# Kernel tuning notes

Measured on AMD Instinct MI355X. Metric: run time of the kernel, lower is better.

## Reference

```python
import jax, jax.numpy as jnp
import numpy as np

# dims (match init_kwargs)
L, CH, PIX, PAT, RC, BD, OUT, B = 64, 16, 256, 64, 32, 64, 10, 256


def setup_inputs() -> dict:
    key = jax.random.key(0)
    ks = jax.random.split(key, 10)
    sd = lambda k, shape, s: jax.random.normal(k, shape, dtype=jnp.float32) * s
    # stds calibrated so each bond-contraction step has ~unit gain (quimb's
    # MPS_rand_state produces normalized states; this mirrors that stability)
    chi_first = sd(ks[0], (RC, CH), 0.70)               # (r, phys)
    chi_mid   = sd(ks[1], (L - 2, RC, RC, CH), 0.70)    # (site, l, r, phys)
    chi_last  = sd(ks[2], (RC, CH, OUT), 0.70 * 0.01)   # (l, phys, out) -- new_ind rand_strength=0.01
    psi_first = sd(ks[3], (BD, PIX), 1.0 / 32)
    psi_mid   = sd(ks[4], (L - 2, BD, BD, PIX), 1.0 / 32)
    psi_last  = sd(ks[5], (BD, PIX), 1.0 / 32)
    phi_first = sd(ks[6], (BD, PAT), 0.125)
    phi_mid   = sd(ks[7], (L - 2, BD, BD, PAT), 0.125)
    phi_last  = sd(ks[8], (BD, PAT), 0.125)
    x = jax.random.normal(ks[9], (B, PAT, PIX, CH), dtype=jnp.float32)
    return dict(x=x, chi_first=chi_first, chi_mid=chi_mid, chi_last=chi_last,
                psi_first=psi_first, psi_mid=psi_mid, psi_last=psi_last,
                phi_first=phi_first, phi_mid=phi_mid, phi_last=phi_last)


def _batched_chain(first, mid, vecs):
    # first: (bond, p); mid: (L-2, l, r, p); vecs: (L, B, p)
    v0 = jnp.einsum('rp,bp->br', first, vecs[0])
    def step(v, wu):
        W, u = wu
        return jnp.einsum('bl,lrp,bp->br', v, W, u), None
    v, _ = jax.lax.scan(step, v0, (mid, vecs[1:-1]))
    return v  # (B, bond)


def reference(x, chi_first, chi_mid, chi_last, psi_first, psi_mid, psi_last,
              phi_first, phi_mid, phi_last):
    Bn, nP, nPix, nCh = x.shape
    idx = jnp.arange(L) % nP  # site -> patch index (identity when L == n_patches)
    # per-site input vectors (contract phys legs of each MPS with data)
    vch = jnp.transpose(x.mean(axis=-2)[:, idx, :], (1, 0, 2))  # (L, B, CH)
    vpx = jnp.transpose(x.mean(axis=-1)[:, idx, :], (1, 0, 2))  # (L, B, PIX)
    # chi chain -> (B, out)
    v_chi = _batched_chain(chi_first, chi_mid, vch)
    chi_out = jnp.einsum('bl,lpo,bp->bo', v_chi, chi_last, vch[-1])
    # psi chain -> (B,)
    v_psi = _batched_chain(psi_first, psi_mid, vpx)
    psi_val = jnp.einsum('bl,lp,bp->b', v_psi, psi_last, vpx[-1])
    # phi chain: one-hot patch positions, batch-independent -> scalar
    e = jax.nn.one_hot(idx, nP, dtype=x.dtype)  # (L, PAT)
    u0 = jnp.einsum('rp,p->r', phi_first, e[0])
    def pstep(v, wu):
        W, u = wu
        return jnp.einsum('l,lrp,p->r', v, W, u), None
    u, _ = jax.lax.scan(pstep, u0, (phi_mid, e[1:-1]))
    phi_val = jnp.einsum('l,lp,p->', u, phi_last, e[-1])
    return chi_out * (psi_val * phi_val)[:, None]  # (B, out)
```

## Files before the change

### kernel.cpp

```cpp
#include <hip/hip_runtime.h>


static inline int imin(int a, int b) { return a < b ? a : b; }

typedef __attribute__((ext_vector_type(4))) float f32x4;
typedef _Float16 f16;
typedef __attribute__((ext_vector_type(8))) _Float16 f16x8;

__global__ __launch_bounds__(256) void k_reduce_x(const float* __restrict__ x,
                                                  float* __restrict__ vch,
                                                  float* __restrict__ vpx,
                                                  f16* __restrict__ vpxf,
                                                  const float* __restrict__ phi_mid,
                                                  float* __restrict__ slices) {
  if (blockIdx.x >= 16384) {
    int i = blockIdx.x - 16384;
    int t = threadIdx.x;
    #pragma unroll
    for (int k = 0; k < 16; ++k) {
      int idx = t + k * 256;
      slices[(size_t)i * 4096 + idx] = phi_mid[((size_t)i * 4096 + idx) * 64 + (i + 1)];
    }
    return;
  }
  int bp = blockIdx.x;
  int b = bp >> 6, s = bp & 63;
  int q = threadIdx.x;
  const float* row = x + ((size_t)bp << 12) + q * 16;
  float4 r0 = *(const float4*)(row);
  float4 r1 = *(const float4*)(row + 4);
  float4 r2 = *(const float4*)(row + 8);
  float4 r3 = *(const float4*)(row + 12);
  float csum = r0.x + r0.y + r0.z + r0.w + r1.x + r1.y + r1.z + r1.w
             + r2.x + r2.y + r2.z + r2.w + r3.x + r3.y + r3.z + r3.w;
  float val = csum * (1.0f / 16.0f);
  if (vpx && (s == 0 || s == 63)) vpx[((size_t)s * 256 + b) * 256 + q] = val;
  if (vpxf && s >= 1 && s <= 62) {
    size_t fa = (size_t)s * 65536
              + (((size_t)(q >> 5) * 16 + (b >> 4)) * 64 + (((q >> 3) & 3) * 16 + (b & 15))) * 8
              + (q & 7);
    vpxf[fa] = (f16)val;
  }

  __shared__ float sc[256][20];
  *(float4*)&sc[q][0]  = r0;
  *(float4*)&sc[q][4]  = r1;
  *(float4*)&sc[q][8]  = r2;
  *(float4*)&sc[q][12] = r3;
  __syncthreads();
  int c = q & 15, g = q >> 4;
  float ps = 0.f;
  #pragma unroll
  for (int k = 0; k < 16; ++k) ps += sc[g * 16 + k][c];
  __shared__ float p2[16][17];
  p2[g][c] = ps;
  __syncthreads();
  if (q < 16) {
    float s2 = 0.f;
    #pragma unroll
    for (int k = 0; k < 16; ++k) s2 += p2[k][q];
    vch[((size_t)s * 256 + b) * 16 + q] = s2 * (1.0f / 256.0f);
  }
}

__device__ __forceinline__ void psi_gemm_tile(const float* __restrict__ W,
                                              const f16* __restrict__ Afg,
                                              f16* __restrict__ Mz,
                                              int lr0, int t,
                                              unsigned char* smem) {
  typedef f16 BArr[2][2][4][64][8];
  BArr& Bf = *reinterpret_cast<BArr*>(smem);
  int lane = t & 63, w = t >> 6;
  int row = t >> 3, kg = t & 7;
  float4 svA0, svA1, svB0, svB1;

  #define LOADPA(p) do {                                                     \
    const float* src = W + (size_t)(lr0 + row) * 256 + ((p) << 6) + kg * 8;  \
    svA0 = *(const float4*)src;                                              \
    svA1 = *(const float4*)(src + 4);                                        \
  } while (0)
  #define LOADPB(p) do {                                                     \
    const float* src = W + (size_t)(lr0 + row) * 256 + ((p) << 6) + kg * 8;  \
    svB0 = *(const float4*)src;                                              \
    svB1 = *(const float4*)(src + 4);                                        \
  } while (0)
  #define WRITEPA(d) do {                                                    \
    float xs[8] = {svA0.x, svA0.y, svA0.z, svA0.w, svA1.x, svA1.y, svA1.z, svA1.w}; \
    f16x8 fv;                                                                \
    _Pragma("unroll")                                                        \
    for (int i = 0; i < 8; ++i) fv[i] = (f16)xs[i];                          \
    int ck = kg >> 2, nt = row >> 4, ln = ((kg & 3) << 4) | (row & 15);      \
    *(f16x8*)&Bf[d][ck][nt][ln][0] = fv;                                     \
  } while (0)
  #define WRITEPB(d) do {                                                    \
    float xs[8] = {svB0.x, svB0.y, svB0.z, svB0.w, svB1.x, svB1.y, svB1.z, svB1.w}; \
    f16x8 fv;                                                                \
    _Pragma("unroll")                                                        \
    for (int i = 0; i < 8; ++i) fv[i] = (f16)xs[i];                          \
    int ck = kg >> 2, nt = row >> 4, ln = ((kg & 3) << 4) | (row & 15);      \
    *(f16x8*)&Bf[d][ck][nt][ln][0] = fv;                                     \
  } while (0)
  #define LOADA(slot, chunk) do {                                            \
    _Pragma("unroll")                                                        \
    for (int mi = 0; mi < 2; ++mi) {                                         \
      size_t fo = ((size_t)(chunk) * 16 + (w * 2 + mi)) * 512 + (size_t)lane * 8; \
      Af[slot][mi] = *(const f16x8*)(Afg + fo);                              \
    }                                                                        \
  } while (0)
  #define COMPUTE(p) do {                                                    \
    _Pragma("unroll")                                                        \
    for (int c = 0; c < 2; ++c) {                                            \
      const int chunk = (p) * 2 + c;                                         \
      const int cur = chunk & 1, nxt = (chunk + 1) & 1;                      \
      if (chunk < 7) LOADA(nxt, chunk + 1);                                  \
      _Pragma("unroll")                                                      \
      for (int n = 0; n < 4; ++n) {                                          \
        f16x8 bf = *(const f16x8*)&Bf[(p) & 1][c][n][lane][0];               \
        _Pragma("unroll")                                                    \
        for (int mi = 0; mi < 2; ++mi) {                                     \
          acc[mi][n] = __builtin_amdgcn_mfma_f32_16x16x32_f16(Af[cur][mi], bf, acc[mi][n], 0, 0, 0); \
        }                                                                    \
      }                                                                      \
    }                                                                        \
  } while (0)

  f32x4 acc[2][4];
  #pragma unroll
  for (int i = 0; i < 2; ++i)
    #pragma unroll
    for (int j = 0; j < 4; ++j) acc[i][j] = (f32x4){0.f, 0.f, 0.f, 0.f};
  f16x8 Af[2][2];

  LOADA(0, 0);
  LOADPA(0);
  LOADPB(1);
  WRITEPA(0);
  __syncthreads();
  LOADPA(2);
  COMPUTE(0);
  WRITEPB(1);
  __syncthreads();
  LOADPB(3);
  COMPUTE(1);
  WRITEPA(0);
  __syncthreads();
  COMPUTE(2);
  WRITEPB(1);
  __syncthreads();
  COMPUTE(3);
  __syncthreads();
  #undef LOADPA
  #undef LOADPB
  #undef WRITEPA
  #undef WRITEPB
  #undef LOADA
  #undef COMPUTE

  int rg = lane >> 4, cidx = lane & 15;
  f16 (*T)[72] = reinterpret_cast<f16 (*)[72]>(smem);
  #pragma unroll
  for (int pass = 0; pass < 2; ++pass) {
    if ((w >> 2) == pass) {
      #pragma unroll
      for (int mi = 0; mi < 2; ++mi) {
        int rowb = (((w & 3) * 2 + mi) * 16) + rg * 4;
        #pragma unroll
        for (int n = 0; n < 4; ++n) {
          #pragma unroll
          for (int r = 0; r < 4; ++r) {
            T[rowb + r][n * 16 + cidx] = (f16)acc[mi][n][r];
          }
        }
      }
    }
    __syncthreads();
    int boff = pass * 128;
    #pragma unroll
    for (int k = 0; k < 2; ++k) {
      int f = t + k * 512;
      int b2 = f >> 3;
      int l8 = (f & 7) * 8;
      *(f16x8*)(Mz + ((size_t)(boff + b2)) * 4096 + lr0 + l8) =
          *(const f16x8*)&T[b2][l8];
    }
    __syncthreads();
  }
}

__global__ __launch_bounds__(512) void k_mega_A(const float* __restrict__ psi_mid,
                                                const f16* __restrict__ vpxf,
                                                f16* __restrict__ M,
                                                const float* __restrict__ chi_mid,
                                                const float* __restrict__ vch,
                                                float* __restrict__ Tc,
                                                const float* __restrict__ slices,
                                                const float* __restrict__ phi_first,
                                                const float* __restrict__ phi_last,
                                                float* __restrict__ phiv) {
  int bx = blockIdx.x;
  int t = threadIdx.x;
  if (bx == 0) {
    int r = t & 63, g = t >> 6;
    __shared__ float u[64];
    __shared__ float part[8][64];
    __shared__ float red[64];
    if (t < 64) u[t] = phi_first[t * 64];
    __syncthreads();
    for (int i2 = 0; i2 < 62; ++i2) {
      float sum = 0.f;
      #pragma unroll
      for (int j = 0; j < 8; ++j) {
        int l = g * 8 + j;
        sum += u[l] * slices[(size_t)i2 * 4096 + l * 64 + r];
      }
      part[g][r] = sum;
      __syncthreads();
      if (g == 0) u[r] = part[0][r] + part[1][r] + part[2][r] + part[3][r]
                       + part[4][r] + part[5][r] + part[6][r] + part[7][r];
      __syncthreads();
    }
    if (t < 64) red[t] = u[t] * phi_last[t * 64 + 63];
    __syncthreads();
    if (t == 0) {
      float s = 0.f;
      for (int l = 0; l < 64; ++l) s += red[l];
      *phiv = s;
    }
  } else if (bx <= 496) {
    int i = bx - 1;
    int z = i >> 3;
    int b0 = (i & 7) * 32;
    __shared__ float uv[32][16];
    if (t < 128) {
      int idx = t * 4;
      int b = idx >> 4, c = idx & 15;
      *(float4*)&uv[b][c] = *(const float4*)(vch + ((size_t)(z + 1) * 256 + b0 + b) * 16 + c);
    }
    __syncthreads();
    #pragma unroll
    for (int k = 0; k < 2; ++k) {
      int idx = t + k * 512;
      int r = idx >> 5, l = idx & 31;
      const float* Wp = chi_mid + ((size_t)z * 1024 + l * 32 + r) * 16;
      float4 w0 = *(const float4*)(Wp);
      float4 w1 = *(const float4*)(Wp + 4);
      float4 w2 = *(const float4*)(Wp + 8);
      float4 w3 = *(const float4*)(Wp + 12);
      for (int b = 0; b < 32; ++b) {
        const float* u = uv[b];
        float d = w0.x * u[0] + w0.y * u[1] + w0.z * u[2] + w0.w * u[3]
                + w1.x * u[4] + w1.y * u[5] + w1.z * u[6] + w1.w * u[7]
                + w2.x * u[8] + w2.y * u[9] + w2.z * u[10] + w2.w * u[11]
                + w3.x * u[12] + w3.y * u[13] + w3.z * u[14] + w3.w * u[15];
        Tc[((size_t)z * 256 + b0 + b) * 1024 + idx] = d;
      }
    }
  } else {
    int idx = bx - 497;
    int z = idx >> 6;
    int lr0 = (idx & 63) * 64;
    __shared__ __align__(16) unsigned char smem[18432];
    psi_gemm_tile(psi_mid + (size_t)z * 4096 * 256,
                  vpxf + (size_t)(z + 1) * 65536,
                  M + (size_t)z * 256 * 4096, lr0, t, smem);
  }
}

__global__ __launch_bounds__(512) void k_mega_B(const float* __restrict__ psi_mid,
                                                const f16* __restrict__ vpxf,
                                                f16* __restrict__ M,
                                                const float* __restrict__ Tc,
                                                const float* __restrict__ vpx,
                                                const float* __restrict__ vch,
                                                const float* __restrict__ psi_first,
                                                const float* __restrict__ chi_first,
                                                const float* __restrict__ chi_last,
                                                float* __restrict__ vpsi,
                                                float* __restrict__ chiout) {
  int bx = blockIdx.x;
  int t = threadIdx.x;
  if (bx < 256) {
    int b = bx;
    int r = t & 63, g = t >> 6;
    __shared__ float vsh[64];
    __shared__ float part[8][64];
    {
      const float* u0 = vpx + (size_t)b * 256;
      const float* pf = psi_first + r * 256 + g * 32;
      float s0 = 0.f;
      #pragma unroll
      for (int p = 0; p < 32; ++p) s0 += pf[p] * u0[g * 32 + p];
      part[g][r] = s0;
      __syncthreads();
      if (g == 0) {
        float sv = 0.f;
        #pragma unroll
        for (int k = 0; k < 8; ++k) sv += part[k][r];
        vsh[r] = sv;
      }
      __syncthreads();
    }
    #define QLOAD(buf, sc) do {                                                \
      const f16* Mb = M + ((size_t)(sc) * 256 + b) * 4096 + r;                 \
      _Pragma("unroll")                                                        \
      for (int j = 0; j < 8; ++j) buf[j] = (float)Mb[(size_t)(g * 8 + j) * 64]; \
    } while (0)
    #define QSTEP(buf) do {                                                    \
      float sum = 0.f;                                                         \
      _Pragma("unroll")                                                        \
      for (int j = 0; j < 8; ++j) sum += vsh[g * 8 + j] * buf[j];              \
      part[g][r] = sum;                                                        \
      __syncthreads();                                                         \
      if (g == 0) {                                                            \
        float sv = 0.f;                                                        \
        _Pragma("unroll")                                                      \
        for (int k = 0; k < 8; ++k) sv += part[k][r];                          \
        vsh[r] = sv;                                                           \
      }                                                                        \
      __syncthreads();                                                         \
    } while (0)
    float bufA[8], bufB[8];
    QLOAD(bufA, 0);
    #pragma unroll 1
    for (int sc = 0; sc < 36; sc += 2) {
      QLOAD(bufB, sc + 1);
      QSTEP(bufA);
      if (sc + 2 < 36) QLOAD(bufA, sc + 2);
      QSTEP(bufB);
    }
    #undef QLOAD
    #undef QSTEP
    if (g == 0) vpsi[b * 64 + r] = vsh[r];
  } else if (bx < 512) {
    if (t >= 64) return;
    int b = bx - 256;
    int lane = t;
    int r = lane & 31, h = lane >> 5;
    float v;
    {
      const float* u0 = vch + (size_t)b * 16;
      const float* cf = chi_first + r * 16;
      float s0 = 0.f;
      #pragma unroll
      for (int c = 0; c < 16; ++c) s0 += cf[c] * u0[c];
      v = s0;
    }
    #define CLOADX(buf, sc) do {                                               \
      const float* Mb = Tc + ((size_t)(sc) * 256 + b) * 1024 + r * 32 + h * 16; \
      *(float4*)&buf[0]  = *(const float4*)(Mb);                               \
      *(float4*)&buf[4]  = *(const float4*)(Mb + 4);                           \
      *(float4*)&buf[8]  = *(const float4*)(Mb + 8);                           \
      *(float4*)&buf[12] = *(const float4*)(Mb + 12);                          \
    } while (0)
    #define CSTEPX(buf) do {                                                   \
      float s0 = 0.f, s1 = 0.f;                                                \
      _Pragma("unroll")                                                        \
      for (int j = 0; j < 8; ++j) {                                            \
        s0 += __shfl(v, h * 16 + 2 * j)     * buf[2 * j];                      \
        s1 += __shfl(v, h * 16 + 2 * j + 1) * buf[2 * j + 1];                  \
      }                                                                        \
      float sum = s0 + s1;                                                     \
      sum += __shfl_xor(sum, 32);                                              \
      v = sum;                                                                 \
    } while (0)
    {
      float mjA[16], mjB[16];
      CLOADX(mjA, 0);
      #pragma unroll 1
      for (int sc = 0; sc < 62; sc += 2) {
        CLOADX(mjB, sc + 1);
        CSTEPX(mjA);
        if (sc + 2 < 62) CLOADX(mjA, sc + 2);
        CSTEPX(mjB);
      }
    }
    #undef CLOADX
    #undef CSTEPX
    const float* u63 = vch + ((size_t)63 * 256 + b) * 16;
    float uc[16];
    #pragma unroll
    for (int c = 0; c < 16; ++c) uc[c] = u63[c];
    for (int o = 0; o < 10; ++o) {
      const float* cl = chi_last + r * 16 * 10 + o;
      float wv = 0.f;
      #pragma unroll
      for (int c = 0; c < 16; ++c) wv += cl[c * 10] * uc[c];
      float p = v * wv;
      #pragma unroll
      for (int m = 32; m > 0; m >>= 1) p += __shfl_xor(p, m);
      if (lane == 0) chiout[b * 10 + o] = p * 0.5f;
    }
  } else {
    int idx = bx - 512;
    int z = 36 + (idx >> 6);
    int lr0 = (idx & 63) * 64;
    __shared__ __align__(16) unsigned char smem[18432];
    psi_gemm_tile(psi_mid + (size_t)z * 4096 * 256,
                  vpxf + (size_t)(z + 1) * 65536,
                  M + (size_t)z * 256 * 4096, lr0, t, smem);
  }
}

__global__ __launch_bounds__(64) void k_chain_tail(const f16* __restrict__ M,
                                                   const float* __restrict__ vpx,
                                                   const float* __restrict__ psi_last,
                                                   const float* __restrict__ chiout,
                                                   const float* __restrict__ phiv,
                                                   const float* __restrict__ vpsi,
                                                   float* __restrict__ out) {
  int b = blockIdx.x;
  int lane = threadIdx.x;
  float v = vpsi[b * 64 + lane];
  #define MLOAD(buf, sc) do {                                                \
    const f16* Mb = M + ((size_t)(36 + (sc)) * 256 + b) * 4096 + lane;       \
    _Pragma("unroll")                                                        \
    for (int l = 0; l < 64; ++l) buf[l] = (float)Mb[(size_t)l * 64];         \
  } while (0)
  #define MSTEP(buf) do {                                                    \
    float s0 = 0.f, s1 = 0.f, s2 = 0.f, s3 = 0.f;                            \
    _Pragma("unroll")                                                        \
    for (int l = 0; l < 16; ++l) {                                           \
      s0 += __shfl(v, 4 * l + 0) * buf[4 * l + 0];                           \
      s1 += __shfl(v, 4 * l + 1) * buf[4 * l + 1];                           \
      s2 += __shfl(v, 4 * l + 2) * buf[4 * l + 2];                           \
      s3 += __shfl(v, 4 * l + 3) * buf[4 * l + 3];                           \
    }                                                                        \
    v = (s0 + s1) + (s2 + s3);                                               \
  } while (0)
  {
    float mvA[64], mvB[64];
    MLOAD(mvA, 0);
    #pragma unroll 1
    for (int sc = 0; sc < 26; sc += 2) {
      MLOAD(mvB, sc + 1);
      MSTEP(mvA);
      if (sc + 2 < 26) MLOAD(mvA, sc + 2);
      MSTEP(mvB);
    }
  }
  #undef MLOAD
  #undef MSTEP
  float acc_p = 0.f;
  #pragma unroll
  for (int pp = 0; pp < 4; ++pp) {
    int p = pp * 64 + lane;
    float pl[64];
    #pragma unroll
    for (int l = 0; l < 64; ++l) pl[l] = psi_last[l * 256 + p];
    float s0 = 0.f, s1 = 0.f, s2 = 0.f, s3 = 0.f;
    #pragma unroll
    for (int l = 0; l < 16; ++l) {
      s0 += __shfl(v, 4 * l + 0) * pl[4 * l + 0];
      s1 += __shfl(v, 4 * l + 1) * pl[4 * l + 1];
      s2 += __shfl(v, 4 * l + 2) * pl[4 * l + 2];
      s3 += __shfl(v, 4 * l + 3) * pl[4 * l + 3];
    }
    float wv = (s0 + s1) + (s2 + s3);
    acc_p += wv * vpx[((size_t)63 * 256 + b) * 256 + p];
  }
  #pragma unroll
  for (int m = 32; m > 0; m >>= 1) acc_p += __shfl_xor(acc_p, m);
  if (lane < 10) out[b * 10 + lane] = chiout[b * 10 + lane] * acc_p * phiv[0];
}

__global__ __launch_bounds__(512) void k_psi_gemm(const float* __restrict__ psi_mid,
                                                  const f16* __restrict__ vpxf,
                                                  f16* __restrict__ M, int s0) {
  int z = blockIdx.z;
  int s = s0 + z;
  int lr0 = blockIdx.x * 64;
  __shared__ __align__(16) unsigned char smem[18432];
  psi_gemm_tile(psi_mid + (size_t)s * 4096 * 256,
                vpxf + (size_t)(s + 1) * 65536,
                M + (size_t)z * 256 * 4096, lr0, threadIdx.x, smem);
}

__global__ __launch_bounds__(256) void k_psi_chain(const f16* __restrict__ M,
                                                   const float* __restrict__ vpx,
                                                   const float* __restrict__ psi_first,
                                                   const float* __restrict__ psi_last,
                                                   float* __restrict__ vpsi,
                                                   float* __restrict__ psiv,
                                                   int nS, int isFirst, int isLast) {
  int b = blockIdx.x;
  int t = threadIdx.x;
  int r = t & 63, g = t >> 6;
  __shared__ float v[64];
  __shared__ float part[4][64];
  __shared__ float red[256];
  if (isFirst) {
    const float* u0 = vpx + (size_t)b * 256;
    float s0 = 0.f;
    for (int p = g * 64; p < g * 64 + 64; ++p) s0 += psi_first[r * 256 + p] * u0[p];
    part[g][r] = s0;
    __syncthreads();
    if (g == 0) v[r] = part[0][r] + part[1][r] + part[2][r] + part[3][r];
    __syncthreads();
  } else {
    if (g == 0) v[r] = vpsi[b * 64 + r];
    __syncthreads();
  }
  for (int sc = 0; sc < nS; ++sc) {
    const f16* Mb = M + ((size_t)sc * 256 + b) * 4096;
    float sum = 0.f;
    #pragma unroll
    for (int j = 0; j < 16; ++j) {
      int l = g * 16 + j;
      sum += v[l] * (float)Mb[l * 64 + r];
    }
    part[g][r] = sum;
    __syncthreads();
    if (g == 0) v[r] = part[0][r] + part[1][r] + part[2][r] + part[3][r];
    __syncthreads();
  }
  if (isLast) {
    float qv = 0.f;
    for (int l = 0; l < 64; ++l) qv += v[l] * psi_last[l * 256 + t];
    red[t] = qv * vpx[((size_t)63 * 256 + b) * 256 + t];
    __syncthreads();
    for (int off = 128; off > 0; off >>= 1) {
      if (t < off) red[t] += red[t + off];
      __syncthreads();
    }
    if (t == 0) psiv[b] = red[0];
  } else {
    if (g == 0) vpsi[b * 64 + r] = v[r];
  }
}

__device__ __forceinline__ void phi_chain_body(const float* __restrict__ slices,
                                               const float* __restrict__ phi_first,
                                               const float* __restrict__ phi_last,
                                               float* __restrict__ phiv) {
  int t = threadIdx.x;
  int r = t & 63, g = t >> 6;
  __shared__ float u[64];
  __shared__ float part[4][64];
  __shared__ float red[64];
  if (t < 64) u[t] = phi_first[t * 64];
  __syncthreads();
  for (int i = 0; i < 62; ++i) {
    float sum = 0.f;
    #pragma unroll
    for (int j = 0; j < 16; ++j) {
      int l = g * 16 + j;
      sum += u[l] * slices[(size_t)i * 4096 + l * 64 + r];
    }
    part[g][r] = sum;
    __syncthreads();
    if (g == 0) u[r] = part[0][r] + part[1][r] + part[2][r] + part[3][r];
    __syncthreads();
  }
  if (t < 64) red[t] = u[t] * phi_last[t * 64 + 63];
  __syncthreads();
  if (t == 0) {
    float s = 0.f;
    for (int l = 0; l < 64; ++l) s += red[l];
    *phiv = s;
  }
}

__global__ __launch_bounds__(256) void k_phi_chain(const float* __restrict__ slices,
                                                   const float* __restrict__ phi_first,
                                                   const float* __restrict__ phi_last,
                                                   float* __restrict__ phiv) {
  phi_chain_body(slices, phi_first, phi_last, phiv);
}

__global__ __launch_bounds__(256) void k_chi_gemm(const float* __restrict__ chi_mid,
                                                  const float* __restrict__ vch,
                                                  float* __restrict__ Tc, int s0,
                                                  int phiBlock,
                                                  const float* __restrict__ slices,
                                                  const float* __restrict__ phi_first,
                                                  const float* __restrict__ phi_last,
                                                  float* __restrict__ phiv) {
  if ((int)blockIdx.x == phiBlock) {
    if (blockIdx.y == 0) phi_chain_body(slices, phi_first, phi_last, phiv);
    return;
  }
  int z = blockIdx.x;
  int s = s0 + z;
  int b0 = blockIdx.y * 32;
  int t = threadIdx.x;
  __shared__ float uv[32][16];
  if (t < 128) {
    int idx = t * 4;
    int b = idx >> 4, c = idx & 15;
    *(float4*)&uv[b][c] = *(const float4*)(vch + ((size_t)(s + 1) * 256 + b0 + b) * 16 + c);
  }
  __syncthreads();
  #pragma unroll
  for (int k = 0; k < 4; ++k) {
    int idx = t + k * 256;
    int r = idx >> 5, l = idx & 31;
    const float* Wp = chi_mid + ((size_t)s * 1024 + l * 32 + r) * 16;
    float4 w0 = *(const float4*)(Wp);
    float4 w1 = *(const float4*)(Wp + 4);
    float4 w2 = *(const float4*)(Wp + 8);
    float4 w3 = *(const float4*)(Wp + 12);
    for (int b = 0; b < 32; ++b) {
      const float* u = uv[b];
      float d = w0.x * u[0] + w0.y * u[1] + w0.z * u[2] + w0.w * u[3]
              + w1.x * u[4] + w1.y * u[5] + w1.z * u[6] + w1.w * u[7]
              + w2.x * u[8] + w2.y * u[9] + w2.z * u[10] + w2.w * u[11]
              + w3.x * u[12] + w3.y * u[13] + w3.z * u[14] + w3.w * u[15];
      Tc[((size_t)z * 256 + b0 + b) * 1024 + idx] = d;
    }
  }
}

__global__ __launch_bounds__(64) void k_chi_chain(const float* __restrict__ Tc,
                                                  const float* __restrict__ chi_first,
                                                  const float* __restrict__ chi_last,
                                                  const float* __restrict__ vch,
                                                  const float* __restrict__ psiv,
                                                  const float* __restrict__ phiv,
                                                  float* __restrict__ vchi,
                                                  float* __restrict__ out,
                                                  int nS, int isFirst, int isLast) {
  int b = blockIdx.x;
  int lane = threadIdx.x;
  int r = lane & 31, h = lane >> 5;
  __shared__ float v[32];
  if (isFirst) {
    if (h == 0) {
      const float* u0 = vch + (size_t)b * 16;
      const float* cf = chi_first + r * 16;
      float s0 = 0.f;
      #pragma unroll
      for (int c = 0; c < 16; ++c) s0 += cf[c] * u0[c];
      v[r] = s0;
    }
  } else {
    if (h == 0) v[r] = vchi[b * 32 + r];
  }
  __syncthreads();
  for (int sc = 0; sc < nS; ++sc) {
    const float* Mb = Tc + ((size_t)sc * 256 + b) * 1024 + r * 32 + h * 16;
    float4 m0 = *(const float4*)(Mb);
    float4 m1 = *(const float4*)(Mb + 4);
    float4 m2 = *(const float4*)(Mb + 8);
    float4 m3 = *(const float4*)(Mb + 12);
    const float* vv = &v[h * 16];
    float sum = m0.x * vv[0] + m0.y * vv[1] + m0.z * vv[2] + m0.w * vv[3]
              + m1.x * vv[4] + m1.y * vv[5] + m1.z * vv[6] + m1.w * vv[7]
              + m2.x * vv[8] + m2.y * vv[9] + m2.z * vv[10] + m2.w * vv[11]
              + m3.x * vv[12] + m3.y * vv[13] + m3.z * vv[14] + m3.w * vv[15];
    sum += __shfl_xor(sum, 32);
    __syncthreads();
    if (h == 0) v[r] = sum;
    __syncthreads();
  }
  if (isLast) {
    const float* u63 = vch + ((size_t)63 * 256 + b) * 16;
    float uc[16];
    #pragma unroll
    for (int c = 0; c < 16; ++c) uc[c] = u63[c];
    float scale = 0.5f * psiv[b] * phiv[0];
    for (int o = 0; o < 10; ++o) {
      const float* cl = chi_last + r * 16 * 10 + o;
      float w = 0.f;
      #pragma unroll
      for (int c = 0; c < 16; ++c) w += cl[c * 10] * uc[c];
      float p = v[r] * w;
      #pragma unroll
      for (int m = 32; m > 0; m >>= 1) p += __shfl_xor(p, m);
      if (lane == 0) out[b * 10 + o] = p * scale;
    }
  } else {
    if (h == 0) vchi[b * 32 + r] = v[r];
  }
}

__global__ __launch_bounds__(256) void k_chi_fused(const float* __restrict__ chi_first,
                                                   const float* __restrict__ chi_mid,
                                                   const float* __restrict__ chi_last,
                                                   const float* __restrict__ vch,
                                                   const float* __restrict__ psiv,
                                                   const float* __restrict__ phiv,
                                                   float* __restrict__ out) {
  int t = threadIdx.x;
  int bl = t >> 6, lg = (t >> 5) & 1, r = t & 31;
  int b = blockIdx.x * 4 + bl;
  __shared__ float v[4][32];
  __shared__ float part[4][2][32];
  if (lg == 0) {
    const float* u0 = vch + (size_t)b * 16;
    float s0 = 0.f;
    #pragma unroll
    for (int c = 0; c < 16; ++c) s0 += chi_first[r * 16 + c] * u0[c];
    v[bl][r] = s0;
  }
  __syncthreads();
  for (int s = 0; s < 62; ++s) {
    const float* u = vch + ((size_t)(s + 1) * 256 + b) * 16;
    float uc[16];
    #pragma unroll
    for (int c = 0; c < 16; ++c) uc[c] = u[c];
    const float* W = chi_mid + (size_t)s * 32 * 32 * 16;
    float sum = 0.f;
    #pragma unroll
    for (int j = 0; j < 16; ++j) {
      int l = lg * 16 + j;
      const float* Wl = W + ((size_t)l * 32 + r) * 16;
      float tt = 0.f;
      #pragma unroll
      for (int c = 0; c < 16; ++c) tt += Wl[c] * uc[c];
      sum += v[bl][l] * tt;
    }
    part[bl][lg][r] = sum;
    __syncthreads();
    if (lg == 0) v[bl][r] = part[bl][0][r] + part[bl][1][r];
    __syncthreads();
  }
  const float* u63 = vch + ((size_t)63 * 256 + b) * 16;
  float uc[16];
  #pragma unroll
  for (int c = 0; c < 16; ++c) uc[c] = u63[c];
  if (r < 10) {
    float acc = 0.f;
    #pragma unroll
    for (int j = 0; j < 16; ++j) {
      int l = lg * 16 + j;
      const float* cl = chi_last + (size_t)l * 16 * 10;
      float tt = 0.f;
      #pragma unroll
      for (int c = 0; c < 16; ++c) tt += cl[c * 10 + r] * uc[c];
      acc += v[bl][l] * tt;
    }
    part[bl][lg][r] = acc;
  }
  __syncthreads();
  if (lg == 0 && r < 10)
    out[b * 10 + r] = (part[bl][0][r] + part[bl][1][r]) * psiv[b] * phiv[0];
}

__global__ __launch_bounds__(256) void k_psi_direct(const float* __restrict__ x,
                                                    const float* __restrict__ psi_mid,
                                                    const float* __restrict__ psi_first,
                                                    const float* __restrict__ psi_last,
                                                    float* __restrict__ psiv) {
  int b = blockIdx.x;
  int t = threadIdx.x;
  int r = t & 63, g = t >> 6;
  __shared__ float u[256];
  __shared__ float v[64];
  __shared__ float part[4][64];
  __shared__ float red[256];
  const float* xb = x + ((size_t)b << 18);
  {
    const float* rw = xb + (size_t)0 * 4096 + t * 16;
    float sm = 0.f;
    #pragma unroll
    for (int c = 0; c < 16; ++c) sm += rw[c];
    u[t] = sm * (1.0f / 16.0f);
  }
  __syncthreads();
  {
    float s0 = 0.f;
    for (int p = g * 64; p < g * 64 + 64; ++p) s0 += psi_first[r * 256 + p] * u[p];
    part[g][r] = s0;
    __syncthreads();
    if (g == 0) v[r] = part[0][r] + part[1][r] + part[2][r] + part[3][r];
  }
  __syncthreads();
  for (int s = 0; s < 62; ++s) {
    __syncthreads();
    {
      const float* rw = xb + (size_t)(s + 1) * 4096 + t * 16;
      float sm = 0.f;
      #pragma unroll
      for (int c = 0; c < 16; ++c) sm += rw[c];
      u[t] = sm * (1.0f / 16.0f);
    }
    __syncthreads();
    const float* W = psi_mid + (size_t)s * 4096 * 256;
    float sum = 0.f;
    for (int l = 0; l < 64; ++l) {
      const float* Wl = W + ((size_t)(l * 64 + r)) * 256 + g * 64;
      float tt = 0.f;
      #pragma unroll 8
      for (int k = 0; k < 64; ++k) tt += Wl[k] * u[g * 64 + k];
      sum += v[l] * tt;
    }
    part[g][r] = sum;
    __syncthreads();
    if (g == 0) v[r] = part[0][r] + part[1][r] + part[2][r] + part[3][r];
    __syncthreads();
  }
  __syncthreads();
  {
    const float* rw = xb + (size_t)63 * 4096 + t * 16;
    float sm = 0.f;
    #pragma unroll
    for (int c = 0; c < 16; ++c) sm += rw[c];
    u[t] = sm * (1.0f / 16.0f);
  }
  __syncthreads();
  float qv = 0.f;
  for (int l = 0; l < 64; ++l) qv += v[l] * psi_last[l * 256 + t];
  red[t] = qv * u[t];
  __syncthreads();
  for (int off = 128; off > 0; off >>= 1) {
    if (t < off) red[t] += red[t + off];
    __syncthreads();
  }
  if (t == 0) psiv[b] = red[0];
}

extern "C" void kernel_launch(void* const* d_in, const int* in_sizes, int n_in,
                              void* d_out, int out_size, void* d_ws, size_t ws_size,
                              hipStream_t stream) {
  const float* x         = (const float*)d_in[0];
  const float* chi_first = (const float*)d_in[1];
  const float* chi_mid   = (const float*)d_in[2];
  const float* chi_last  = (const float*)d_in[3];
  const float* psi_first = (const float*)d_in[4];
  const float* psi_mid   = (const float*)d_in[5];
  const float* psi_last  = (const float*)d_in[6];
  const float* phi_first = (const float*)d_in[7];
  const float* phi_mid   = (const float*)d_in[8];
  const float* phi_last  = (const float*)d_in[9];
  float* out = (float*)d_out;
  float* ws  = (float*)d_ws;

  size_t wsf = ws_size / 4;
  size_t off = 0;
  float* vch    = ws + off; off += (size_t)64 * 256 * 16;
  float* psiv   = ws + off; off += 256;
  float* chiout = ws + off; off += 2560;
  float* phisl  = ws + off; off += (size_t)62 * 64 * 64;
  float* phiv   = ws + off; off += 16;
  float* vpsi   = ws + off; off += (size_t)64 * 256;
  float* vchi   = ws + off; off += (size_t)32 * 256;
  float* vpx    = ws + off; off += (size_t)64 * 256 * 256;
  f16* vpxf = (f16*)(ws + off); off += (size_t)64 * 65536 / 2;
  f16* Mbuf = (f16*)(ws + off);
  size_t needMh  = (size_t)62 * 256 * 4096;
  float* Tcbuf = (float*)(Mbuf + needMh);
  size_t needTc = (size_t)62 * 256 * 1024;
  size_t bytes_needed = off * 4 + needMh * 2 + needTc * 4;

  if (ws_size >= bytes_needed) {
    k_reduce_x<<<16384 + 62, 256, 0, stream>>>(x, vch, vpx, vpxf,
                                               phi_mid, phisl);
    k_mega_A<<<497 + 2304, 512, 0, stream>>>(psi_mid, vpxf, Mbuf,
                                             chi_mid, vch, Tcbuf,
                                             phisl, phi_first, phi_last, phiv);
    k_mega_B<<<512 + 1664, 512, 0, stream>>>(psi_mid, vpxf, Mbuf,
                                             Tcbuf, vpx, vch, psi_first,
                                             chi_first, chi_last, vpsi, chiout);
    k_chain_tail<<<256, 64, 0, stream>>>(Mbuf, vpx, psi_last, chiout, phiv,
                                         vpsi, out);
  } else {
    size_t avail_b = (ws_size > off * 4) ? ws_size - off * 4 : 0;
    int C = (int)(avail_b / ((size_t)256 * 4096 * 2));
    if (C > 62) C = 62;
    int Cc = (int)(avail_b / ((size_t)256 * 1024 * 4));
    if (Cc > 62) Cc = 62;
    if (C >= 1) {
      k_reduce_x<<<16384 + 62, 256, 0, stream>>>(x, vch, vpx, vpxf,
                                                 phi_mid, phisl);
      int done = 0;
      while (done < 62) {
        int c = imin(C, 62 - done);
        k_psi_gemm<<<dim3(64, 1, c), 512, 0, stream>>>(psi_mid, vpxf, Mbuf, done);
        k_psi_chain<<<256, 256, 0, stream>>>(Mbuf, vpx, psi_first, psi_last,
                                             vpsi, psiv, c, (done == 0) ? 1 : 0,
                                             (done + c == 62) ? 1 : 0);
        done += c;
      }
      done = 0;
      while (done < 62) {
        int c = imin(Cc, 62 - done);
        int phiBlk = (done == 0) ? c : -1;
        int gx = (done == 0) ? (c + 1) : c;
        k_chi_gemm<<<dim3(gx, 8), 256, 0, stream>>>(chi_mid, vch, (float*)Mbuf, done, phiBlk,
                                                    phisl, phi_first, phi_last, phiv);
        k_chi_chain<<<256, 64, 0, stream>>>((float*)Mbuf, chi_first, chi_last, vch,
                                            psiv, phiv, vchi, out, c,
                                            (done == 0) ? 1 : 0,
                                            (done + c == 62) ? 1 : 0);
        done += c;
      }
    } else {
      k_reduce_x<<<16384 + 62, 256, 0, stream>>>(x, vch, nullptr, nullptr,
                                                 phi_mid, phisl);
      k_psi_direct<<<256, 256, 0, stream>>>(x, psi_mid, psi_first, psi_last, psiv);
      k_phi_chain<<<1, 256, 0, stream>>>(phisl, phi_first, phi_last, phiv);
      k_chi_fused<<<64, 256, 0, stream>>>(chi_first, chi_mid, chi_last, vch, psiv, phiv, out);
    }
  }
}
```

Measured before the change: 248.4 us.

## Run psi chain per-wavefront with shuffles and pack 8 batches per block

```diff
diff --git a/kernel.cpp b/kernel.cpp
--- a/kernel.cpp
+++ b/kernel.cpp
@@ -279,62 +279,52 @@
                                                 float* __restrict__ chiout) {
   int bx = blockIdx.x;
   int t = threadIdx.x;
-  if (bx < 256) {
-    int b = bx;
-    int r = t & 63, g = t >> 6;
-    __shared__ float vsh[64];
-    __shared__ float part[8][64];
+  int bl = t >> 6, lane = t & 63;
+  if (bx < 32) {
+    int b = bx * 8 + bl;
+    float v;
     {
       const float* u0 = vpx + (size_t)b * 256;
-      const float* pf = psi_first + r * 256 + g * 32;
-      float s0 = 0.f;
-      #pragma unroll
-      for (int p = 0; p < 32; ++p) s0 += pf[p] * u0[g * 32 + p];
-      part[g][r] = s0;
-      __syncthreads();
-      if (g == 0) {
-        float sv = 0.f;
-        #pragma unroll
-        for (int k = 0; k < 8; ++k) sv += part[k][r];
-        vsh[r] = sv;
+      const float* pf = psi_first + lane * 256;
+      float s0 = 0.f, s1 = 0.f, s2 = 0.f, s3 = 0.f;
+      for (int p = 0; p < 256; p += 4) {
+        s0 += pf[p] * u0[p];   s1 += pf[p + 1] * u0[p + 1];
+        s2 += pf[p + 2] * u0[p + 2]; s3 += pf[p + 3] * u0[p + 3];
       }
-      __syncthreads();
-    }
-    #define QLOAD(buf, sc) do {                                                \
-      const f16* Mb = M + ((size_t)(sc) * 256 + b) * 4096 + r;                 \
+      v = (s0 + s1) + (s2 + s3);
+    }
+    #define MLOAD1(buf, sc) do {                                               \
+      const f16* Mb = M + ((size_t)(sc) * 256 + b) * 4096 + lane;              \
       _Pragma("unroll")                                                        \
-      for (int j = 0; j < 8; ++j) buf[j] = (float)Mb[(size_t)(g * 8 + j) * 64]; \
+      for (int l = 0; l < 64; ++l) buf[l] = (float)Mb[(size_t)l * 64];         \
     } while (0)
-    #define QSTEP(buf) do {                                                    \
-      float sum = 0.f;                                                         \
+    #define MSTEP1(buf) do {                                                   \
+      float s0 = 0.f, s1 = 0.f, s2 = 0.f, s3 = 0.f;                            \
       _Pragma("unroll")                                                        \
-      for (int j = 0; j < 8; ++j) sum += vsh[g * 8 + j] * buf[j];              \
-      part[g][r] = sum;                                                        \
-      __syncthreads();                                                         \
-      if (g == 0) {                                                            \
-        float sv = 0.f;                                                        \
-        _Pragma("unroll")                                                      \
-        for (int k = 0; k < 8; ++k) sv += part[k][r];                          \
-        vsh[r] = sv;                                                           \
+      for (int l = 0; l < 16; ++l) {                                           \
+        s0 += __shfl(v, 4 * l + 0) * buf[4 * l + 0];                           \
+        s1 += __shfl(v, 4 * l + 1) * buf[4 * l + 1];                           \
+        s2 += __shfl(v, 4 * l + 2) * buf[4 * l + 2];                           \
+        s3 += __shfl(v, 4 * l + 3) * buf[4 * l + 3];                           \
       }                                                                        \
-      __syncthreads();                                                         \
+      v = (s0 + s1) + (s2 + s3);                                               \
     } while (0)
-    float bufA[8], bufB[8];
-    QLOAD(bufA, 0);
-    #pragma unroll 1
-    for (int sc = 0; sc < 36; sc += 2) {
-      QLOAD(bufB, sc + 1);
-      QSTEP(bufA);
-      if (sc + 2 < 36) QLOAD(bufA, sc + 2);
-      QSTEP(bufB);
-    }
-    #undef QLOAD
-    #undef QSTEP
-    if (g == 0) vpsi[b * 64 + r] = vsh[r];
-  } else if (bx < 512) {
-    if (t >= 64) return;
-    int b = bx - 256;
-    int lane = t;
+    {
+      float mvA[64], mvB[64];
+      MLOAD1(mvA, 0);
+      #pragma unroll 1
+      for (int sc = 0; sc < 36; sc += 2) {
+        MLOAD1(mvB, sc + 1);
+        MSTEP1(mvA);
+        if (sc + 2 < 36) MLOAD1(mvA, sc + 2);
+        MSTEP1(mvB);
+      }
+    }
+    #undef MLOAD1
+    #undef MSTEP1
+    vpsi[b * 64 + lane] = v;
+  } else if (bx < 64) {
+    int b = (bx - 32) * 8 + bl;
     int r = lane & 31, h = lane >> 5;
     float v;
     {
@@ -391,7 +381,7 @@
       if (lane == 0) chiout[b * 10 + o] = p * 0.5f;
     }
   } else {
-    int idx = bx - 512;
+    int idx = bx - 64;
     int z = 36 + (idx >> 6);
     int lr0 = (idx & 63) * 64;
     __shared__ __align__(16) unsigned char smem[18432];
@@ -848,9 +838,9 @@
     k_mega_A<<<497 + 2304, 512, 0, stream>>>(psi_mid, vpxf, Mbuf,
                                              chi_mid, vch, Tcbuf,
                                              phisl, phi_first, phi_last, phiv);
-    k_mega_B<<<512 + 1664, 512, 0, stream>>>(psi_mid, vpxf, Mbuf,
-                                             Tcbuf, vpx, vch, psi_first,
-                                             chi_first, chi_last, vpsi, chiout);
+    k_mega_B<<<64 + 1664, 512, 0, stream>>>(psi_mid, vpxf, Mbuf,
+                                            Tcbuf, vpx, vch, psi_first,
+                                            chi_first, chi_last, vpsi, chiout);
     k_chain_tail<<<256, 64, 0, stream>>>(Mbuf, vpx, psi_last, chiout, phiv,
                                          vpsi, out);
   } else {
```

Result: slower. 350.5 us (+41.1%).
